# Kernel tuning notes

Measured on AMD Instinct MI355X. Metric: run time of the kernel, lower is better.

Reference implementation:

```python
import jax, jax.numpy as jnp
import numpy as np

B, S, D, C = 64, 576, 768, 200


def setup_inputs() -> dict:
    key = jax.random.key(0)
    k1, k2, k3, k4 = jax.random.split(key, 4)
    return {
        "patch_tokens": jax.random.normal(k1, (B, S, D), dtype=jnp.float32),
        "class_token": jax.random.normal(k2, (B, D), dtype=jnp.float32),
        "attn_w": jax.random.normal(k3, (C, D), dtype=jnp.float32) * (1.0 / np.sqrt(D)),
        "attn_b": jnp.zeros((C,), dtype=jnp.float32),
        "gc_w": jax.random.normal(k4, (C, D), dtype=jnp.float32) * (1.0 / np.sqrt(D)),
        "gc_b": jnp.zeros((C,), dtype=jnp.float32),
        "lam": jnp.ones((1,), dtype=jnp.float32),
    }


def reference(patch_tokens, class_token, attn_w, attn_b, gc_w, gc_b, lam):
    # patch_tokens: (B,S,D). The torch module reshapes S to HxW, but the mean
    # over (H,W) equals the mean over S, so we stay in token layout.
    _, S_, D_ = patch_tokens.shape
    # Global classifier: (B,C)
    global_scores = class_token @ gc_w.T + gc_b
    # Per-class 1x1 conv == per-class linear projection over tokens: (B,C,S)
    att = jax.nn.sigmoid(
        jnp.einsum("bsd,cd->bcs", patch_tokens, attn_w) + attn_b[None, :, None]
    )
    # mean over spatial (S) then mean over channels (D):
    # mean_d mean_s (att * feat) == einsum / (S*D)
    attention_scores = jnp.einsum("bcs,bsd->bc", att, patch_tokens) / (S_ * D_)
    return global_scores + lam[0] * attention_scores
```

## Files before the change

kernel.cpp:

```cpp
#include <hip/hip_runtime.h>
#include <math.h>

#define Bsz  64
#define Ssz  576
#define Dsz  768
#define Csz  200
#define NPAD 208
#define MT   48
#define NKT  12
#define NCH  48

typedef float f32x4 __attribute__((ext_vector_type(4)));

#define AS_GLOBAL __attribute__((address_space(1)))
#define AS_LDS    __attribute__((address_space(3)))

__device__ inline void gload16(const void* g, void* l) {
    __builtin_amdgcn_global_load_lds((const AS_GLOBAL unsigned int*)g,
                                     (AS_LDS unsigned int*)l, 16, 0, 0);
}

__global__ __launch_bounds__(256) void prep_w8(const float* __restrict__ W,
                                               unsigned int* __restrict__ Wq) {
    const int i   = blockIdx.x * 256 + threadIdx.x;
    const int row = i / 192;
    const int col = (i % 192) * 4;
    unsigned int w = 0;
    if (row < Csz) {
        const float4 v = *(const float4*)(W + (size_t)row * Dsz + col);
        w = __builtin_amdgcn_cvt_pk_fp8_f32(v.x, v.y, 0u, false);
        w = __builtin_amdgcn_cvt_pk_fp8_f32(v.z, v.w, w, true);
    } else if (row == Csz) {
        w = 0x38383838u;
    }
    Wq[i] = w;
}

__global__ __launch_bounds__(256) void gc_kernel(
    const float* __restrict__ ct, const float* __restrict__ gw,
    const float* __restrict__ gb, float* __restrict__ out) {
    const int b    = blockIdx.x;
    const int wv   = threadIdx.x >> 6;
    const int lane = threadIdx.x & 63;
    const int c    = blockIdx.y * 4 + wv;
    const float* wr = gw + (size_t)c * Dsz + lane * 12;
    const float* cr = ct + (size_t)b * Dsz + lane * 12;
    float s = 0.f;
#pragma unroll
    for (int j = 0; j < 3; ++j) {
        const float4 w = *(const float4*)(wr + 4 * j);
        const float4 x = *(const float4*)(cr + 4 * j);
        s += w.x * x.x + w.y * x.y + w.z * x.z + w.w * x.w;
    }
#pragma unroll
    for (int off = 32; off > 0; off >>= 1) s += __shfl_down(s, off, 64);
    if (lane == 0) out[b * Csz + c] = s + gb[c];
}

__global__ __launch_bounds__(192, 1) void attn_kernel(
    const float* __restrict__ X,
    const unsigned char* __restrict__ Wq,
    const float* __restrict__ attn_b,
    const float* __restrict__ lam,
    float* __restrict__ out)
{
    __shared__ unsigned char sW[NPAD * NCH * 16];

    const int tid  = threadIdx.x;
    const int lane = tid & 63;
    const int w    = tid >> 6;
    const int m    = lane & 15;
    const int q    = lane >> 4;
    const int rowbase = blockIdx.x * MT;
    const int bidx    = blockIdx.x / 12;

    const float* xp = X + (size_t)(rowbase + w * 16 + m) * Dsz + q * 8;

    f32x4 xa[4][4];
#pragma unroll
    for (int kt = 0; kt < 4; ++kt) {
#pragma unroll
        for (int j = 0; j < 4; ++j)
            xa[kt][j] = *(const f32x4*)(xp + kt * 64 + (j >> 1) * 32 + (j & 1) * 4);
    }

#pragma unroll 4
    for (int j = 0; j < 52; ++j) {
        const int g = w * 52 + j;
        const int s = g * 64 + lane;
        const int c = s / NPAD;
        const int r = s - c * NPAD;
        gload16(Wq + (size_t)r * Dsz + c * 16, &sW[(size_t)(g * 64) * 16]);
    }

    f32x4 acc[13];
#pragma unroll
    for (int t = 0; t < 13; ++t) acc[t] = (f32x4){0.f, 0.f, 0.f, 0.f};

    const int wbase = m * 16 + (q & 1) * 8 + (q >> 1) * 3328;

    __syncthreads();

#pragma unroll
    for (int kt = 0; kt < NKT; ++kt) {
        const int slot = kt & 3;
#pragma unroll
        for (int k2 = 0; k2 < 2; ++k2) {
            const f32x4 alo = xa[slot][k2 * 2];
            const f32x4 ahi = xa[slot][k2 * 2 + 1];
            union { long l; unsigned int u[2]; } A;
            A.u[0] = __builtin_amdgcn_cvt_pk_fp8_f32(alo.x, alo.y, 0u, false);
            A.u[0] = __builtin_amdgcn_cvt_pk_fp8_f32(alo.z, alo.w, A.u[0], true);
            A.u[1] = __builtin_amdgcn_cvt_pk_fp8_f32(ahi.x, ahi.y, 0u, false);
            A.u[1] = __builtin_amdgcn_cvt_pk_fp8_f32(ahi.z, ahi.w, A.u[1], true);
            const unsigned char* wb = &sW[(kt * 4 + k2 * 2) * 3328 + wbase];
#pragma unroll
            for (int t = 0; t < 13; ++t) {
                const long Bf = *(const long*)(wb + t * 256);
                acc[t] = __builtin_amdgcn_mfma_f32_16x16x32_fp8_fp8(A.l, Bf, acc[t], 0, 0, 0);
            }
        }
        if (kt + 4 < NKT) {
#pragma unroll
            for (int j = 0; j < 4; ++j)
                xa[slot][j] = *(const f32x4*)(xp + (kt + 4) * 64 + (j >> 1) * 32 + (j & 1) * 4);
        }
    }

    float rsv[4];
#pragma unroll
    for (int r = 0; r < 4; ++r) rsv[r] = __shfl(acc[12][r], (lane & 48) + 8, 64);

    const float scale = lam[0] * (1.f / ((float)Ssz * (float)Dsz));
#pragma unroll
    for (int t = 0; t < 13; ++t) {
        const int c = t * 16 + m;
        if (c < Csz) {
            const float bias = attn_b[c];
            float s = 0.f;
#pragma unroll
            for (int r = 0; r < 4; ++r)
                s += rsv[r] / (1.f + __expf(-(acc[t][r] + bias)));
            s += __shfl_xor(s, 16, 64);
            s += __shfl_xor(s, 32, 64);
            if (q == 0) atomicAdd(&out[bidx * Csz + c], s * scale);
        }
    }
}

extern "C" void kernel_launch(void* const* d_in, const int* in_sizes, int n_in,
                              void* d_out, int out_size, void* d_ws, size_t ws_size,
                              hipStream_t stream) {
    const float* X   = (const float*)d_in[0];
    const float* ct  = (const float*)d_in[1];
    const float* aw  = (const float*)d_in[2];
    const float* ab  = (const float*)d_in[3];
    const float* gw  = (const float*)d_in[4];
    const float* gb  = (const float*)d_in[5];
    const float* lam = (const float*)d_in[6];
    float* out = (float*)d_out;
    unsigned char* Wq = (unsigned char*)d_ws;

    prep_w8<<<(NPAD * Dsz / 4) / 256, 256, 0, stream>>>(aw, (unsigned int*)Wq);
    gc_kernel<<<dim3(Bsz, Csz / 4), 256, 0, stream>>>(ct, gw, gb, out);
    attn_kernel<<<(Bsz * Ssz) / MT, 192, 0, stream>>>(X, Wq, ab, lam, out);
}
```

Before: 240.0 us.

## Pre-swizzle FP8 weights into MFMA fragment order and stream from global instead of LDS

The prep kernel now writes the FP8 attention weights in the exact per-lane MFMA B-fragment order, so each lane reads a 16-byte vector per tile straight from global/L2. This removes the per-block bulk copy of the whole weight matrix into LDS and the barrier before compute. With no LDS and a shallower X prefetch, launch bounds now allow up to three blocks per CU. The trade-off is repeated weight reads from L2 in every block, plus fewer X loads kept in flight.

```diff
diff --git a/kernel.cpp b/kernel.cpp
--- a/kernel.cpp
+++ b/kernel.cpp
@@ -5,35 +5,37 @@
 #define Ssz  576
 #define Dsz  768
 #define Csz  200
-#define NPAD 208
 #define MT   48
 #define NKT  12
-#define NCH  48
 
 typedef float f32x4 __attribute__((ext_vector_type(4)));
-
-#define AS_GLOBAL __attribute__((address_space(1)))
-#define AS_LDS    __attribute__((address_space(3)))
-
-__device__ inline void gload16(const void* g, void* l) {
-    __builtin_amdgcn_global_load_lds((const AS_GLOBAL unsigned int*)g,
-                                     (AS_LDS unsigned int*)l, 16, 0, 0);
-}
+typedef long  lx2   __attribute__((ext_vector_type(2)));
 
 __global__ __launch_bounds__(256) void prep_w8(const float* __restrict__ W,
-                                               unsigned int* __restrict__ Wq) {
-    const int i   = blockIdx.x * 256 + threadIdx.x;
-    const int row = i / 192;
-    const int col = (i % 192) * 4;
-    unsigned int w = 0;
+                                               unsigned long long* __restrict__ Wq) {
+    const int i  = blockIdx.x * 256 + threadIdx.x;
+    const int h  = i & 1;
+    const int j  = i >> 1;
+    const int l  = j & 63;
+    const int r2 = j >> 6;
+    const int t  = r2 % 13;
+    const int kt = r2 / 13;
+    const int q  = l >> 4, m = l & 15;
+    const int row = t * 16 + m;
+    const int col = kt * 64 + h * 32 + ((q >> 1) << 4) + ((q & 1) << 3);
+    unsigned long long v = 0ull;
     if (row < Csz) {
-        const float4 v = *(const float4*)(W + (size_t)row * Dsz + col);
-        w = __builtin_amdgcn_cvt_pk_fp8_f32(v.x, v.y, 0u, false);
-        w = __builtin_amdgcn_cvt_pk_fp8_f32(v.z, v.w, w, true);
+        const float4 a = *(const float4*)(W + (size_t)row * Dsz + col);
+        const float4 b = *(const float4*)(W + (size_t)row * Dsz + col + 4);
+        unsigned int lo = __builtin_amdgcn_cvt_pk_fp8_f32(a.x, a.y, 0u, false);
+        lo = __builtin_amdgcn_cvt_pk_fp8_f32(a.z, a.w, lo, true);
+        unsigned int hi = __builtin_amdgcn_cvt_pk_fp8_f32(b.x, b.y, 0u, false);
+        hi = __builtin_amdgcn_cvt_pk_fp8_f32(b.z, b.w, hi, true);
+        v = ((unsigned long long)hi << 32) | (unsigned long long)lo;
     } else if (row == Csz) {
-        w = 0x38383838u;
+        v = 0x3838383838383838ull;
     }
-    Wq[i] = w;
+    Wq[i] = v;
 }
 
 __global__ __launch_bounds__(256) void gc_kernel(
@@ -57,15 +59,13 @@
     if (lane == 0) out[b * Csz + c] = s + gb[c];
 }
 
-__global__ __launch_bounds__(192, 1) void attn_kernel(
+__global__ __launch_bounds__(192, 3) void attn_kernel(
     const float* __restrict__ X,
     const unsigned char* __restrict__ Wq,
     const float* __restrict__ attn_b,
     const float* __restrict__ lam,
     float* __restrict__ out)
 {
-    __shared__ unsigned char sW[NPAD * NCH * 16];
-
     const int tid  = threadIdx.x;
     const int lane = tid & 63;
     const int w    = tid >> 6;
@@ -75,55 +75,61 @@
     const int bidx    = blockIdx.x / 12;
 
     const float* xp = X + (size_t)(rowbase + w * 16 + m) * Dsz + q * 8;
+    const unsigned char* wp = Wq + lane * 16;
 
-    f32x4 xa[4][4];
+    f32x4 xa[2][4];
 #pragma unroll
-    for (int kt = 0; kt < 4; ++kt) {
+    for (int kt = 0; kt < 2; ++kt) {
 #pragma unroll
         for (int j = 0; j < 4; ++j)
             xa[kt][j] = *(const f32x4*)(xp + kt * 64 + (j >> 1) * 32 + (j & 1) * 4);
-    }
-
-#pragma unroll 4
-    for (int j = 0; j < 52; ++j) {
-        const int g = w * 52 + j;
-        const int s = g * 64 + lane;
-        const int c = s / NPAD;
-        const int r = s - c * NPAD;
-        gload16(Wq + (size_t)r * Dsz + c * 16, &sW[(size_t)(g * 64) * 16]);
     }
 
     f32x4 acc[13];
 #pragma unroll
     for (int t = 0; t < 13; ++t) acc[t] = (f32x4){0.f, 0.f, 0.f, 0.f};
 
-    const int wbase = m * 16 + (q & 1) * 8 + (q >> 1) * 3328;
+#pragma unroll
+    for (int kt = 0; kt < NKT; ++kt) {
+        const int slot = kt & 1;
+        lx2 wf[13];
+#pragma unroll
+        for (int t = 0; t < 13; ++t)
+            wf[t] = *(const lx2*)(wp + (size_t)(kt * 13 + t) * 1024);
 
-    __syncthreads();
+        f32x4 xn[4];
+        if (kt + 2 < NKT) {
+#pragma unroll
+            for (int j = 0; j < 4; ++j)
+                xn[j] = *(const f32x4*)(xp + (kt + 2) * 64 + (j >> 1) * 32 + (j & 1) * 4);
+        }
+
+        union { long l; unsigned int u[2]; } A0, A1;
+        {
+            const f32x4 alo = xa[slot][0], ahi = xa[slot][1];
+            A0.u[0] = __builtin_amdgcn_cvt_pk_fp8_f32(alo.x, alo.y, 0u, false);
+            A0.u[0] = __builtin_amdgcn_cvt_pk_fp8_f32(alo.z, alo.w, A0.u[0], true);
+            A0.u[1] = __builtin_amdgcn_cvt_pk_fp8_f32(ahi.x, ahi.y, 0u, false);
+            A0.u[1] = __builtin_amdgcn_cvt_pk_fp8_f32(ahi.z, ahi.w, A0.u[1], true);
+        }
+        {
+            const f32x4 alo = xa[slot][2], ahi = xa[slot][3];
+            A1.u[0] = __builtin_amdgcn_cvt_pk_fp8_f32(alo.x, alo.y, 0u, false);
+            A1.u[0] = __builtin_amdgcn_cvt_pk_fp8_f32(alo.z, alo.w, A1.u[0], true);
+            A1.u[1] = __builtin_amdgcn_cvt_pk_fp8_f32(ahi.x, ahi.y, 0u, false);
+            A1.u[1] = __builtin_amdgcn_cvt_pk_fp8_f32(ahi.z, ahi.w, A1.u[1], true);
+        }
 
 #pragma unroll
-    for (int kt = 0; kt < NKT; ++kt) {
-        const int slot = kt & 3;
+        for (int t = 0; t < 13; ++t)
+            acc[t] = __builtin_amdgcn_mfma_f32_16x16x32_fp8_fp8(A0.l, wf[t][0], acc[t], 0, 0, 0);
 #pragma unroll
-        for (int k2 = 0; k2 < 2; ++k2) {
-            const f32x4 alo = xa[slot][k2 * 2];
-            const f32x4 ahi = xa[slot][k2 * 2 + 1];
-            union { long l; unsigned int u[2]; } A;
-            A.u[0] = __builtin_amdgcn_cvt_pk_fp8_f32(alo.x, alo.y, 0u, false);
-            A.u[0] = __builtin_amdgcn_cvt_pk_fp8_f32(alo.z, alo.w, A.u[0], true);
-            A.u[1] = __builtin_amdgcn_cvt_pk_fp8_f32(ahi.x, ahi.y, 0u, false);
-            A.u[1] = __builtin_amdgcn_cvt_pk_fp8_f32(ahi.z, ahi.w, A.u[1], true);
-            const unsigned char* wb = &sW[(kt * 4 + k2 * 2) * 3328 + wbase];
+        for (int t = 0; t < 13; ++t)
+            acc[t] = __builtin_amdgcn_mfma_f32_16x16x32_fp8_fp8(A1.l, wf[t][1], acc[t], 0, 0, 0);
+
+        if (kt + 2 < NKT) {
 #pragma unroll
-            for (int t = 0; t < 13; ++t) {
-                const long Bf = *(const long*)(wb + t * 256);
-                acc[t] = __builtin_amdgcn_mfma_f32_16x16x32_fp8_fp8(A.l, Bf, acc[t], 0, 0, 0);
-            }
-        }
-        if (kt + 4 < NKT) {
-#pragma unroll
-            for (int j = 0; j < 4; ++j)
-                xa[slot][j] = *(const f32x4*)(xp + (kt + 4) * 64 + (j >> 1) * 32 + (j & 1) * 4);
+            for (int j = 0; j < 4; ++j) xa[slot][j] = xn[j];
         }
     }
 
@@ -159,9 +165,9 @@
     const float* gb  = (const float*)d_in[5];
     const float* lam = (const float*)d_in[6];
     float* out = (float*)d_out;
-    unsigned char* Wq = (unsigned char*)d_ws;
+    unsigned long long* Wq = (unsigned long long*)d_ws;
 
-    prep_w8<<<(NPAD * Dsz / 4) / 256, 256, 0, stream>>>(aw, (unsigned int*)Wq);
+    prep_w8<<<(NKT * 13 * 64 * 2) / 256, 256, 0, stream>>>(aw, Wq);
     gc_kernel<<<dim3(Bsz, Csz / 4), 256, 0, stream>>>(ct, gw, gb, out);
-    attn_kernel<<<(Bsz * Ssz) / MT, 192, 0, stream>>>(X, Wq, ab, lam, out);
+    attn_kernel<<<(Bsz * Ssz) / MT, 192, 0, stream>>>(X, (const unsigned char*)Wq, ab, lam, out);
 }
```

New measurement: 205.8 us. 14.2% less time.
